# Kernel optimization log

Hardware: AMD Instinct MI355X
Metric: run time of the kernel (lower is better)

Reference implementation:

```python
import jax, jax.numpy as jnp
import numpy as np

DIM_IN, DIM_Q, DIM_V = 1024, 1024, 1024
B, S = 4, 2048
NEG_INF = 1.0e9


def setup_inputs() -> dict:
    key = jax.random.key(0)
    ks = jax.random.split(key, 11)
    c_q = (6.0 / (DIM_IN + DIM_Q)) ** 0.5
    c_v = (6.0 / (DIM_IN + DIM_V)) ** 0.5
    b_bound = 1.0 / np.sqrt(DIM_IN)  # torch Linear default bias init
    return {
        "query": jax.random.normal(ks[0], (B, S, DIM_IN), jnp.float32),
        "key": jax.random.normal(ks[1], (B, S, DIM_IN), jnp.float32),
        "value": jax.random.normal(ks[2], (B, S, DIM_IN), jnp.float32),
        "mask": jax.random.randint(ks[3], (B, S, S), 0, 2).astype(bool),
        "Wq": jax.random.uniform(ks[4], (DIM_Q, DIM_IN), jnp.float32, -c_q, c_q),
        "bq": jax.random.uniform(ks[5], (DIM_Q,), jnp.float32, -b_bound, b_bound),
        "Wk": jax.random.uniform(ks[6], (DIM_Q, DIM_IN), jnp.float32, -c_q, c_q),
        "bk": jax.random.uniform(ks[7], (DIM_Q,), jnp.float32, -b_bound, b_bound),
        "Wv": jax.random.uniform(ks[8], (DIM_V, DIM_IN), jnp.float32, -c_v, c_v),
        "bv": jax.random.uniform(ks[9], (DIM_V,), jnp.float32, -b_bound, b_bound),
    }


def reference(query, key, value, mask, Wq, bq, Wk, bk, Wv, bv):
    q = jnp.einsum("bsd,qd->bsq", query, Wq) + bq  # [B,S,dim_q]
    k = jnp.einsum("bsd,qd->bsq", key, Wk) + bk    # [B,S,dim_q]
    v = jnp.einsum("bsd,vd->bsv", value, Wv) + bv  # [B,S,dim_v]
    scale = 1.0 / jnp.sqrt(jnp.asarray(q.shape[-1], q.dtype))
    scores = jnp.einsum("bqd,bkd->bqk", q, k) * scale  # [B,S,S]
    scores = jnp.where(mask, -NEG_INF, scores)
    affinity = jax.nn.softmax(scores, axis=-1)
    out = jnp.einsum("bqk,bkv->bqv", affinity, v)  # [B,S,dim_v]
    return out
```

## Files before the change

### kernel.cpp

```cpp
#include <hip/hip_runtime.h>

#define BB 4
#define SS 2048
#define DD 1024

typedef __attribute__((ext_vector_type(8))) short short8;
typedef __attribute__((ext_vector_type(4))) float f32x4;

__device__ __forceinline__ unsigned short f2b(float f) {
  unsigned u = __builtin_bit_cast(unsigned, f);
  u += 0x7fffu + ((u >> 16) & 1u);
  return (unsigned short)(u >> 16);
}
__device__ __forceinline__ float b2f(unsigned short us) {
  unsigned u = (unsigned)us << 16;
  return __builtin_bit_cast(float, u);
}

__device__ __forceinline__ void gl2lds16(const void* g, void* l) {
  __builtin_amdgcn_global_load_lds(
      (__attribute__((address_space(1))) unsigned int*)(void*)(size_t)(uintptr_t)g,
      (__attribute__((address_space(3))) unsigned int*)l, 16, 0, 0);
}

__global__ __launch_bounds__(256) void cvt_all(
    const float* __restrict__ q, const float* __restrict__ k, const float* __restrict__ v,
    const float* __restrict__ wq, const float* __restrict__ wk, const float* __restrict__ wv,
    unsigned short* __restrict__ qo, unsigned short* __restrict__ ko, unsigned short* __restrict__ vo,
    unsigned short* __restrict__ wqo, unsigned short* __restrict__ wko, unsigned short* __restrict__ wvo) {
  const int z = blockIdx.z;
  const float* s;
  unsigned short* d;
  size_t i;
  if (blockIdx.x < 4096) {
    s = z == 0 ? q : (z == 1 ? k : v);
    d = z == 0 ? qo : (z == 1 ? ko : vo);
    i = (size_t)blockIdx.x * 2048 + threadIdx.x * 8;
  } else {
    s = z == 0 ? wq : (z == 1 ? wk : wv);
    d = z == 0 ? wqo : (z == 1 ? wko : wvo);
    i = (size_t)(blockIdx.x - 4096) * 2048 + threadIdx.x * 8;
  }
  float4 a = *(const float4*)(s + i);
  float4 b = *(const float4*)(s + i + 4);
  union { unsigned short us[8]; uint4 v4; } o;
  o.us[0] = f2b(a.x); o.us[1] = f2b(a.y); o.us[2] = f2b(a.z); o.us[3] = f2b(a.w);
  o.us[4] = f2b(b.x); o.us[5] = f2b(b.y); o.us[6] = f2b(b.z); o.us[7] = f2b(b.w);
  *(uint4*)(d + i) = o.v4;
}

enum { EPI_BIAS_COL = 0, EPI_BIAS_ROW = 1, EPI_SCORE = 2, EPI_OUT = 3 };

template <int EPI>
__global__ __launch_bounds__(256, 2) void gemm_bt(
    const unsigned short* __restrict__ A, int lda, long long aBatch,
    const unsigned short* __restrict__ Bm, int ldb, long long bBatch,
    void* __restrict__ Cv, int ldc, long long cBatch,
    int K,
    const float* __restrict__ bias,
    const float* __restrict__ bias2,
    float scale) {
  __shared__ unsigned short sA[2][128 * 32];
  __shared__ unsigned short sB[2][128 * 32];
  const int tid  = threadIdx.x;
  const int wave = tid >> 6;
  const int lane = tid & 63;
  const int l15  = lane & 15;
  const int quad = lane >> 4;
  const int waveR = wave >> 1, waveC = wave & 1;
  const int bm = blockIdx.x * 128;
  const int bn = blockIdx.y * 128;
  const int z  = blockIdx.z;
  A  += (long long)z * aBatch;
  Bm += (long long)z * bBatch;

  const unsigned short* gA0 = A  + (size_t)(bm + (tid >> 2)) * lda + (tid & 3) * 8;
  const unsigned short* gA1 = gA0 + (size_t)64 * lda;
  const unsigned short* gB0 = Bm + (size_t)(bn + (tid >> 2)) * ldb + (tid & 3) * 8;
  const unsigned short* gB1 = gB0 + (size_t)64 * ldb;
  const int ldsOff = wave * 64 * 8;

  f32x4 acc[4][4] = {};

  const int aro = (waveR * 64 + l15) * 32 + quad * 8;
  const int bro = (waveC * 64 + l15) * 32 + quad * 8;

  auto stage = [&](int c, int kt) {
    unsigned short* lA = sA[c] + ldsOff;
    unsigned short* lB = sB[c] + ldsOff;
    gl2lds16(gA0 + kt, lA);
    gl2lds16(gA1 + kt, lA + 256 * 8);
    gl2lds16(gB0 + kt, lB);
    gl2lds16(gB1 + kt, lB + 256 * 8);
  };

  stage(0, 0);
  int cur = 0;

  for (int kt = 0; kt < K; kt += 32) {
    __syncthreads();
    short8 af[4], bf[4];
#pragma unroll
    for (int i = 0; i < 4; ++i) af[i] = *(const short8*)(sA[cur] + aro + i * 16 * 32);
#pragma unroll
    for (int j = 0; j < 4; ++j) bf[j] = *(const short8*)(sB[cur] + bro + j * 16 * 32);
    __builtin_amdgcn_sched_barrier(0);
    if (kt + 32 < K) stage(cur ^ 1, kt + 32);
    __builtin_amdgcn_sched_barrier(0);
#pragma unroll
    for (int i = 0; i < 4; ++i)
#pragma unroll
      for (int j = 0; j < 4; ++j)
        acc[i][j] = __builtin_amdgcn_mfma_f32_16x16x32_bf16(af[i], bf[j], acc[i][j], 0, 0, 0);
    cur ^= 1;
  }

  const int r0 = bm + waveR * 64 + quad * 4;
  const int c0 = bn + waveC * 64 + l15;

  if constexpr (EPI == EPI_SCORE) {
    unsigned short* Cz = (unsigned short*)Cv + (long long)z * cBatch;
#pragma unroll
    for (int i = 0; i < 4; ++i)
#pragma unroll
      for (int r = 0; r < 4; ++r) {
        int row = r0 + i * 16 + r;
#pragma unroll
        for (int j = 0; j < 4; ++j) {
          int col = c0 + j * 16;
          Cz[(size_t)row * ldc + col] = f2b(acc[i][j][r] * scale);
        }
      }
  } else if constexpr (EPI == EPI_OUT) {
    float* Cz = (float*)Cv + (long long)z * cBatch;
#pragma unroll
    for (int i = 0; i < 4; ++i)
#pragma unroll
      for (int r = 0; r < 4; ++r) {
        int row = r0 + i * 16 + r;
#pragma unroll
        for (int j = 0; j < 4; ++j) {
          int col = c0 + j * 16;
          Cz[(size_t)row * ldc + col] = acc[i][j][r];
        }
      }
  } else {
    const float* bp = (z == 0) ? bias : bias2;
    unsigned short* Cz = (unsigned short*)Cv + (long long)z * cBatch;
#pragma unroll
    for (int i = 0; i < 4; ++i)
#pragma unroll
      for (int r = 0; r < 4; ++r) {
        int row = r0 + i * 16 + r;
#pragma unroll
        for (int j = 0; j < 4; ++j) {
          int col = c0 + j * 16;
          float v = acc[i][j][r] + (EPI == EPI_BIAS_COL ? bp[col] : bp[row]);
          Cz[(size_t)row * ldc + col] = f2b(v);
        }
      }
  }
}

__global__ __launch_bounds__(256) void softmax_rows(const unsigned short* __restrict__ Sc,
                                                    const void* __restrict__ mask,
                                                    unsigned short* __restrict__ P) {
  const size_t r = blockIdx.x;
  const unsigned short* src = Sc + r * SS;
  unsigned short* dst = P + r * SS;
  const int tid = threadIdx.x;
  const int wave = tid >> 6, lane = tid & 63;
  __shared__ int anyv[4];
  __shared__ float red[8];

  unsigned pw = ((const unsigned*)mask)[tid];
  unsigned long long bal = __ballot(pw > 1u);
  if (lane == 0) anyv[wave] = (bal != 0ULL) ? 1 : 0;
  __syncthreads();
  const bool isU8 = (anyv[0] | anyv[1] | anyv[2] | anyv[3]) != 0;

  unsigned mbits = 0;
  if (isU8) {
    uint2 v = *(const uint2*)((const unsigned char*)mask + r * SS + tid * 8);
#pragma unroll
    for (int j = 0; j < 4; ++j) {
      mbits |= (((v.x >> (8 * j)) & 0xffu) ? 1u : 0u) << j;
      mbits |= (((v.y >> (8 * j)) & 0xffu) ? 1u : 0u) << (j + 4);
    }
  } else {
    const uint4* p = (const uint4*)((const int*)mask + r * SS + tid * 8);
    uint4 a = p[0], b = p[1];
    mbits = (a.x ? 1u : 0u) | ((a.y ? 1u : 0u) << 1) | ((a.z ? 1u : 0u) << 2) |
            ((a.w ? 1u : 0u) << 3) | ((b.x ? 1u : 0u) << 4) | ((b.y ? 1u : 0u) << 5) |
            ((b.z ? 1u : 0u) << 6) | ((b.w ? 1u : 0u) << 7);
  }

  union { unsigned short us[8]; uint4 v; } in;
  in.v = *(const uint4*)(src + tid * 8);
  float xs[8];
#pragma unroll
  for (int k = 0; k < 8; ++k)
    xs[k] = ((mbits >> k) & 1u) ? -1.0e9f : b2f(in.us[k]);
  float mx = xs[0];
#pragma unroll
  for (int k = 1; k < 8; ++k) mx = fmaxf(mx, xs[k]);
#pragma unroll
  for (int o = 32; o; o >>= 1) mx = fmaxf(mx, __shfl_xor(mx, o));
  if (lane == 0) red[wave] = mx;
  __syncthreads();
  mx = fmaxf(fmaxf(red[0], red[1]), fmaxf(red[2], red[3]));
  float e[8], s = 0.f;
#pragma unroll
  for (int k = 0; k < 8; ++k) { e[k] = __expf(xs[k] - mx); s += e[k]; }
#pragma unroll
  for (int o = 32; o; o >>= 1) s += __shfl_xor(s, o);
  if (lane == 0) red[4 + wave] = s;
  __syncthreads();
  s = (red[4] + red[5]) + (red[6] + red[7]);
  float inv = 1.0f / s;
  union { unsigned short us[8]; uint4 v; } o;
#pragma unroll
  for (int k = 0; k < 8; ++k) o.us[k] = f2b(e[k] * inv);
  *(uint4*)(dst + tid * 8) = o.v;
}

extern "C" void kernel_launch(void* const* d_in, const int* in_sizes, int n_in,
                              void* d_out, int out_size, void* d_ws, size_t ws_size,
                              hipStream_t stream) {
  const float* query = (const float*)d_in[0];
  const float* key   = (const float*)d_in[1];
  const float* value = (const float*)d_in[2];
  const void*  mask  = d_in[3];
  const float* Wq = (const float*)d_in[4];
  const float* bq = (const float*)d_in[5];
  const float* Wk = (const float*)d_in[6];
  const float* bk = (const float*)d_in[7];
  const float* Wv = (const float*)d_in[8];
  const float* bv = (const float*)d_in[9];
  float* out = (float*)d_out;

  char* ws = (char*)d_ws;
  const size_t MB = 1024 * 1024;
  unsigned short* qin = (unsigned short*)(ws + 0 * MB);
  unsigned short* kin = (unsigned short*)(ws + 16 * MB);
  unsigned short* vin = (unsigned short*)(ws + 32 * MB);
  unsigned short* Wqb = (unsigned short*)(ws + 48 * MB);
  unsigned short* Wkb = (unsigned short*)(ws + 50 * MB);
  unsigned short* Wvb = (unsigned short*)(ws + 52 * MB);
  unsigned short* qb  = (unsigned short*)(ws + 54 * MB);
  unsigned short* kb  = (unsigned short*)(ws + 70 * MB);
  unsigned short* vT  = (unsigned short*)(ws + 86 * MB);
  unsigned short* Sc  = (unsigned short*)(ws + 102 * MB);
  unsigned short* P   = (unsigned short*)(ws + 134 * MB);

  dim3 blk(256);

  cvt_all<<<dim3(4608, 1, 3), blk, 0, stream>>>(
      query, key, value, Wq, Wk, Wv, qin, kin, vin, Wqb, Wkb, Wvb);

  gemm_bt<EPI_BIAS_COL><<<dim3(64, 8, 2), blk, 0, stream>>>(
      qin, 1024, 8388608LL, Wqb, 1024, 1048576LL, qb, 1024, 8388608LL,
      1024, bq, bk, 0.f);

  gemm_bt<EPI_BIAS_ROW><<<dim3(8, 64, 1), blk, 0, stream>>>(
      Wvb, 1024, 0, vin, 1024, 0, vT, 8192, 0, 1024, bv, bv, 0.f);

  gemm_bt<EPI_SCORE><<<dim3(16, 16, BB), blk, 0, stream>>>(
      qb, 1024, (long long)SS * 1024, kb, 1024, (long long)SS * 1024,
      Sc, SS, (long long)SS * SS, 1024, nullptr, nullptr, 0.03125f);

  softmax_rows<<<dim3(BB * SS), blk, 0, stream>>>(Sc, mask, P);

  gemm_bt<EPI_OUT><<<dim3(16, 8, BB), blk, 0, stream>>>(
      P, SS, (long long)SS * SS, vT, 8192, (long long)SS,
      out, 1024, (long long)SS * 1024, SS, nullptr, nullptr, 1.f);
}
```

Baseline: 367.8 us.

## Fuse fp32-to-bf16 conversion into a single combined QKV projection kernel

```diff
diff --git a/kernel.cpp b/kernel.cpp
--- a/kernel.cpp
+++ b/kernel.cpp
@@ -23,43 +23,124 @@
       (__attribute__((address_space(3))) unsigned int*)l, 16, 0, 0);
 }
 
-__global__ __launch_bounds__(256) void cvt_all(
-    const float* __restrict__ q, const float* __restrict__ k, const float* __restrict__ v,
-    const float* __restrict__ wq, const float* __restrict__ wk, const float* __restrict__ wv,
-    unsigned short* __restrict__ qo, unsigned short* __restrict__ ko, unsigned short* __restrict__ vo,
-    unsigned short* __restrict__ wqo, unsigned short* __restrict__ wko, unsigned short* __restrict__ wvo) {
-  const int z = blockIdx.z;
-  const float* s;
-  unsigned short* d;
-  size_t i;
-  if (blockIdx.x < 4096) {
-    s = z == 0 ? q : (z == 1 ? k : v);
-    d = z == 0 ? qo : (z == 1 ? ko : vo);
-    i = (size_t)blockIdx.x * 2048 + threadIdx.x * 8;
-  } else {
-    s = z == 0 ? wq : (z == 1 ? wk : wv);
-    d = z == 0 ? wqo : (z == 1 ? wko : wvo);
-    i = (size_t)(blockIdx.x - 4096) * 2048 + threadIdx.x * 8;
-  }
-  float4 a = *(const float4*)(s + i);
-  float4 b = *(const float4*)(s + i + 4);
-  union { unsigned short us[8]; uint4 v4; } o;
+__device__ __forceinline__ uint4 cvt8(float4 a, float4 b) {
+  union { unsigned short us[8]; uint4 v; } o;
   o.us[0] = f2b(a.x); o.us[1] = f2b(a.y); o.us[2] = f2b(a.z); o.us[3] = f2b(a.w);
   o.us[4] = f2b(b.x); o.us[5] = f2b(b.y); o.us[6] = f2b(b.z); o.us[7] = f2b(b.w);
-  *(uint4*)(d + i) = o.v4;
-}
-
-enum { EPI_BIAS_COL = 0, EPI_BIAS_ROW = 1, EPI_SCORE = 2, EPI_OUT = 3 };
+  return o.v;
+}
+
+__global__ __launch_bounds__(256, 2) void proj_f32(
+    const float* __restrict__ query, const float* __restrict__ key,
+    const float* __restrict__ value,
+    const float* __restrict__ Wq, const float* __restrict__ Wk,
+    const float* __restrict__ Wv,
+    const float* __restrict__ bq, const float* __restrict__ bk,
+    const float* __restrict__ bv,
+    unsigned short* __restrict__ qkb,
+    unsigned short* __restrict__ vT) {
+  __shared__ unsigned short sA[2][128 * 32];
+  __shared__ unsigned short sB[2][128 * 32];
+  const int tid  = threadIdx.x;
+  const int wave = tid >> 6;
+  const int lane = tid & 63;
+  const int l15  = lane & 15;
+  const int quad = lane >> 4;
+  const int waveR = wave >> 1, waveC = wave & 1;
+  const int z = blockIdx.z;
+
+  const float* Ap; const float* Bp; const float* bp;
+  unsigned short* C; int ldc, bm, bn; bool rowb;
+  if (z == 2) {
+    Ap = Wv; Bp = value; bp = bv; C = vT; ldc = 8192; rowb = true;
+    bm = blockIdx.y * 128; bn = blockIdx.x * 128;
+  } else {
+    Ap = z ? key : query; Bp = z ? Wk : Wq; bp = z ? bk : bq;
+    C = qkb + (size_t)z * 8388608; ldc = 1024; rowb = false;
+    bm = blockIdx.x * 128; bn = blockIdx.y * 128;
+  }
+
+  const int srow = tid >> 2, cgrp = (tid & 3) * 8;
+  const float* gA0 = Ap + (size_t)(bm + srow) * 1024 + cgrp;
+  const float* gA1 = gA0 + (size_t)64 * 1024;
+  const float* gB0 = Bp + (size_t)(bn + srow) * 1024 + cgrp;
+  const float* gB1 = gB0 + (size_t)64 * 1024;
+
+  f32x4 acc[4][4] = {};
+  const int aro = (waveR * 64 + l15) * 32 + quad * 8;
+  const int bro = (waveC * 64 + l15) * 32 + quad * 8;
+
+  {
+    float4 a0 = *(const float4*)gA0, a1 = *(const float4*)(gA0 + 4);
+    float4 a2 = *(const float4*)gA1, a3 = *(const float4*)(gA1 + 4);
+    float4 b0 = *(const float4*)gB0, b1 = *(const float4*)(gB0 + 4);
+    float4 b2 = *(const float4*)gB1, b3 = *(const float4*)(gB1 + 4);
+    *(uint4*)(sA[0] + tid * 8)        = cvt8(a0, a1);
+    *(uint4*)(sA[0] + tid * 8 + 2048) = cvt8(a2, a3);
+    *(uint4*)(sB[0] + tid * 8)        = cvt8(b0, b1);
+    *(uint4*)(sB[0] + tid * 8 + 2048) = cvt8(b2, b3);
+  }
+  int cur = 0;
+
+  for (int kt = 0; kt < 1024; kt += 32) {
+    __syncthreads();
+    short8 af[4], bf[4];
+#pragma unroll
+    for (int i = 0; i < 4; ++i) af[i] = *(const short8*)(sA[cur] + aro + i * 16 * 32);
+#pragma unroll
+    for (int j = 0; j < 4; ++j) bf[j] = *(const short8*)(sB[cur] + bro + j * 16 * 32);
+    __builtin_amdgcn_sched_barrier(0);
+    const bool pf = (kt + 32) < 1024;
+    float4 a0, a1, a2, a3, b0, b1, b2, b3;
+    if (pf) {
+      const int o = kt + 32;
+      a0 = *(const float4*)(gA0 + o); a1 = *(const float4*)(gA0 + o + 4);
+      a2 = *(const float4*)(gA1 + o); a3 = *(const float4*)(gA1 + o + 4);
+      b0 = *(const float4*)(gB0 + o); b1 = *(const float4*)(gB0 + o + 4);
+      b2 = *(const float4*)(gB1 + o); b3 = *(const float4*)(gB1 + o + 4);
+    }
+    __builtin_amdgcn_sched_barrier(0);
+#pragma unroll
+    for (int i = 0; i < 4; ++i)
+#pragma unroll
+      for (int j = 0; j < 4; ++j)
+        acc[i][j] = __builtin_amdgcn_mfma_f32_16x16x32_bf16(af[i], bf[j], acc[i][j], 0, 0, 0);
+    __builtin_amdgcn_sched_barrier(0);
+    if (pf) {
+      unsigned short* dA = sA[cur ^ 1];
+      unsigned short* dB = sB[cur ^ 1];
+      *(uint4*)(dA + tid * 8)        = cvt8(a0, a1);
+      *(uint4*)(dA + tid * 8 + 2048) = cvt8(a2, a3);
+      *(uint4*)(dB + tid * 8)        = cvt8(b0, b1);
+      *(uint4*)(dB + tid * 8 + 2048) = cvt8(b2, b3);
+    }
+    cur ^= 1;
+  }
+
+  const int r0 = bm + waveR * 64 + quad * 4;
+  const int c0 = bn + waveC * 64 + l15;
+#pragma unroll
+  for (int i = 0; i < 4; ++i)
+#pragma unroll
+    for (int r = 0; r < 4; ++r) {
+      int row = r0 + i * 16 + r;
+#pragma unroll
+      for (int j = 0; j < 4; ++j) {
+        int col = c0 + j * 16;
+        float v = acc[i][j][r] + (rowb ? bp[row] : bp[col]);
+        C[(size_t)row * ldc + col] = f2b(v);
+      }
+    }
+}
+
+enum { EPI_SCORE = 2, EPI_OUT = 3 };
 
 template <int EPI>
 __global__ __launch_bounds__(256, 2) void gemm_bt(
     const unsigned short* __restrict__ A, int lda, long long aBatch,
     const unsigned short* __restrict__ Bm, int ldb, long long bBatch,
     void* __restrict__ Cv, int ldc, long long cBatch,
-    int K,
-    const float* __restrict__ bias,
-    const float* __restrict__ bias2,
-    float scale) {
+    int K, float scale) {
   __shared__ unsigned short sA[2][128 * 32];
   __shared__ unsigned short sB[2][128 * 32];
   const int tid  = threadIdx.x;
@@ -131,7 +212,7 @@
           Cz[(size_t)row * ldc + col] = f2b(acc[i][j][r] * scale);
         }
       }
-  } else if constexpr (EPI == EPI_OUT) {
+  } else {
     float* Cz = (float*)Cv + (long long)z * cBatch;
 #pragma unroll
     for (int i = 0; i < 4; ++i)
@@ -142,21 +223,6 @@
         for (int j = 0; j < 4; ++j) {
           int col = c0 + j * 16;
           Cz[(size_t)row * ldc + col] = acc[i][j][r];
-        }
-      }
-  } else {
-    const float* bp = (z == 0) ? bias : bias2;
-    unsigned short* Cz = (unsigned short*)Cv + (long long)z * cBatch;
-#pragma unroll
-    for (int i = 0; i < 4; ++i)
-#pragma unroll
-      for (int r = 0; r < 4; ++r) {
-        int row = r0 + i * 16 + r;
-#pragma unroll
-        for (int j = 0; j < 4; ++j) {
-          int col = c0 + j * 16;
-          float v = acc[i][j][r] + (EPI == EPI_BIAS_COL ? bp[col] : bp[row]);
-          Cz[(size_t)row * ldc + col] = f2b(v);
         }
       }
   }
@@ -241,12 +307,6 @@
 
   char* ws = (char*)d_ws;
   const size_t MB = 1024 * 1024;
-  unsigned short* qin = (unsigned short*)(ws + 0 * MB);
-  unsigned short* kin = (unsigned short*)(ws + 16 * MB);
-  unsigned short* vin = (unsigned short*)(ws + 32 * MB);
-  unsigned short* Wqb = (unsigned short*)(ws + 48 * MB);
-  unsigned short* Wkb = (unsigned short*)(ws + 50 * MB);
-  unsigned short* Wvb = (unsigned short*)(ws + 52 * MB);
   unsigned short* qb  = (unsigned short*)(ws + 54 * MB);
   unsigned short* kb  = (unsigned short*)(ws + 70 * MB);
   unsigned short* vT  = (unsigned short*)(ws + 86 * MB);
@@ -255,23 +315,16 @@
 
   dim3 blk(256);
 
-  cvt_all<<<dim3(4608, 1, 3), blk, 0, stream>>>(
-      query, key, value, Wq, Wk, Wv, qin, kin, vin, Wqb, Wkb, Wvb);
-
-  gemm_bt<EPI_BIAS_COL><<<dim3(64, 8, 2), blk, 0, stream>>>(
-      qin, 1024, 8388608LL, Wqb, 1024, 1048576LL, qb, 1024, 8388608LL,
-      1024, bq, bk, 0.f);
-
-  gemm_bt<EPI_BIAS_ROW><<<dim3(8, 64, 1), blk, 0, stream>>>(
-      Wvb, 1024, 0, vin, 1024, 0, vT, 8192, 0, 1024, bv, bv, 0.f);
+  proj_f32<<<dim3(64, 8, 3), blk, 0, stream>>>(
+      query, key, value, Wq, Wk, Wv, bq, bk, bv, qb, vT);
 
   gemm_bt<EPI_SCORE><<<dim3(16, 16, BB), blk, 0, stream>>>(
       qb, 1024, (long long)SS * 1024, kb, 1024, (long long)SS * 1024,
-      Sc, SS, (long long)SS * SS, 1024, nullptr, nullptr, 0.03125f);
+      Sc, SS, (long long)SS * SS, 1024, 0.03125f);
 
   softmax_rows<<<dim3(BB * SS), blk, 0, stream>>>(Sc, mask, P);
 
   gemm_bt<EPI_OUT><<<dim3(16, 8, BB), blk, 0, stream>>>(
       P, SS, (long long)SS * SS, vT, 8192, (long long)SS,
-      out, 1024, (long long)SS * 1024, SS, nullptr, nullptr, 1.f);
-}
+      out, 1024, (long long)SS * 1024, SS, 1.f);
+}
```

New measurement: 429.9 us. 1.17x slower.
